# Performance work log

Hardware: AMD Instinct MI355X
Metric: run time of the kernel (lower is better)

Reference implementation:

```python
import jax, jax.numpy as jnp
import numpy as np

NUM_HEADS = 16


def setup_inputs() -> dict:
    key = jax.random.key(0)
    k1, k2, k3, k4 = jax.random.split(key, 4)
    B, N, C = 4, 2048, 1024
    x = jax.random.normal(k1, (B, N, C), dtype=jnp.float32)
    # binary window mask (0/1) as float, shape [B, N, 1]
    mWin = jnp.round(jax.random.uniform(k2, (B, N, 1), dtype=jnp.float32))
    qkv_w = jax.random.normal(k3, (3 * C, C), dtype=jnp.float32) * (C ** -0.5)
    proj_w = jax.random.normal(k4, (C, C), dtype=jnp.float32) * (C ** -0.5)
    proj_b = jnp.zeros((C,), dtype=jnp.float32)
    return {"x": x, "mWin": mWin, "qkv_w": qkv_w, "proj_w": proj_w, "proj_b": proj_b}


def reference(x, mWin, qkv_w, proj_w, proj_b):
    B, N, C = x.shape
    H = NUM_HEADS
    hd = C // H
    scale = hd ** -0.5
    qkv = (x @ qkv_w.T).reshape(B, N, 3, H, hd).transpose(2, 0, 3, 1, 4)
    q, k, v = qkv[0], qkv[1], qkv[2]
    q = q * scale
    m = mWin[:, None]              # [B,1,N,1], broadcasts over heads
    q = q * m
    k = k * m
    v = v * m
    attn = jax.nn.softmax(jnp.einsum('bhqd,bhkd->bhqk', q, k), axis=-1)
    out = jnp.einsum('bhqk,bhkd->bhqd', attn, v)  # [B,H,N,hd]
    out = out.transpose(0, 2, 1, 3).reshape(B, N, C)
    # mx = ((m @ m^T) @ m) = m * sum(m^2) since m is [N,1]; identical math, no NxN buffer
    mx = mWin * jnp.sum(mWin * mWin, axis=1, keepdims=True)  # [B,N,1]
    out = out / (mx + 1e-6)
    return out @ proj_w.T + proj_b
```

## Files before the change

### kernel.cpp

```cpp
#include <hip/hip_runtime.h>

typedef __attribute__((ext_vector_type(8))) short short8v;
typedef __attribute__((ext_vector_type(4))) float f32x4;
typedef __attribute__((ext_vector_type(4))) unsigned short us4;

#define MFMA(a,b,c) __builtin_amdgcn_mfma_f32_16x16x32_bf16(a,b,c,0,0,0)

__device__ __forceinline__ unsigned short f2b(float f){
  unsigned int u = __float_as_uint(f);
  u += 0x7fffu + ((u >> 16) & 1u);
  return (unsigned short)(u >> 16);
}

__device__ __forceinline__ void gll16(const void* g, void* l){
  __builtin_amdgcn_global_load_lds((const __attribute__((address_space(1))) void*)g,
                                   (__attribute__((address_space(3))) void*)l, 16, 0, 0);
}

__device__ __forceinline__ unsigned int cvtpk(float lo, float hi){
  unsigned int r;
  asm("v_cvt_pk_bf16_f32 %0, %1, %2" : "=v"(r) : "v"(lo), "v"(hi));
  return r;
}
__device__ __forceinline__ void pl32swap(unsigned int &a, unsigned int &b){
  asm("v_permlane32_swap_b32 %0, %1" : "+v"(a), "+v"(b));
}
__device__ __forceinline__ void pl16swap(unsigned int &a, unsigned int &b){
  asm("v_permlane16_swap_b32 %0, %1" : "+v"(a), "+v"(b));
}

union U8 { unsigned int u[4]; short8v v; };

__global__ __launch_bounds__(256) void prep_k(
    const float* __restrict__ x, const float* __restrict__ qkv_w,
    const float* __restrict__ proj_w, const float* __restrict__ mWin,
    unsigned short* __restrict__ xb, unsigned short* __restrict__ wqkvb,
    unsigned short* __restrict__ wprojb, float* __restrict__ cnt){
  int blk = blockIdx.x, tid = threadIdx.x;
  const float* src; unsigned short* dst; int base;
  if (blk < 8192){ src = x; dst = xb; base = 0; }
  else if (blk < 11264){ src = qkv_w; dst = wqkvb; base = 8192; }
  else if (blk < 12288){ src = proj_w; dst = wprojb; base = 11264; }
  else {
    int b = blk - 12288;
    float s = 0.f;
    for (int i = tid; i < 2048; i += 256){ float m = mWin[b*2048 + i]; s += m*m; }
    #pragma unroll
    for (int o = 32; o >= 1; o >>= 1) s += __shfl_xor(s, o, 64);
    if ((tid & 63) == 0) atomicAdd(&cnt[b], s);
    return;
  }
  int i = (blk - base)*256 + tid;
  float4 v = reinterpret_cast<const float4*>(src)[i];
  us4 o; o.x = f2b(v.x); o.y = f2b(v.y); o.z = f2b(v.z); o.w = f2b(v.w);
  reinterpret_cast<us4*>(dst)[i] = o;
}

__global__ __launch_bounds__(256,2) void qkv_gemm(
    const unsigned short* __restrict__ xb,
    const unsigned short* __restrict__ wb,
    const float* __restrict__ mWin,
    unsigned short* __restrict__ qb,
    unsigned short* __restrict__ kb,
    unsigned short* __restrict__ vb)
{
  __shared__ unsigned short As[128*64];
  __shared__ unsigned short Bs[128*64];
  int lin = blockIdx.x;
  int swz = (lin & 7) * 192 + (lin >> 3);
  int tM = swz & 63, tN = swz >> 6;
  int tid = threadIdx.x, lane = tid & 63, wv = tid >> 6;
  int lr = lane & 15, lg = lane >> 4;

  const unsigned short* ga[4]; const unsigned short* gbp[4];
  char* lA[4]; char* lB[4];
  #pragma unroll
  for (int c = 0; c < 4; ++c){
    int o = c*4096 + wv*1024 + lane*16;
    int row = o >> 7, cole = (o & 127) >> 1;
    ga[c]  = xb + (tM*128 + row)*1024 + cole;
    gbp[c] = wb + (tN*128 + row)*1024 + cole;
    lA[c] = (char*)As + c*4096 + wv*1024;
    lB[c] = (char*)Bs + c*4096 + wv*1024;
  }

  f32x4 acc[4][4];
  #pragma unroll
  for (int i = 0; i < 4; ++i)
    #pragma unroll
    for (int j = 0; j < 4; ++j) acc[i][j] = (f32x4){0.f,0.f,0.f,0.f};

  int wr = (wv >> 1) * 64, wc = (wv & 1) * 64;

  for (int it = 0; it < 16; ++it){
    #pragma unroll
    for (int c = 0; c < 4; ++c){
      gll16(ga[c]  + it*64, lA[c]);
      gll16(gbp[c] + it*64, lB[c]);
    }
    __syncthreads();
    short8v af[4][2], bf[4][2];
    #pragma unroll
    for (int mi = 0; mi < 4; ++mi)
      #pragma unroll
      for (int ks = 0; ks < 2; ++ks)
        af[mi][ks] = *(const short8v*)&As[(wr + mi*16 + lr)*64 + ks*32 + lg*8];
    #pragma unroll
    for (int ni = 0; ni < 4; ++ni)
      #pragma unroll
      for (int ks = 0; ks < 2; ++ks)
        bf[ni][ks] = *(const short8v*)&Bs[(wc + ni*16 + lr)*64 + ks*32 + lg*8];
    #pragma unroll
    for (int mi = 0; mi < 4; ++mi)
      #pragma unroll
      for (int ni = 0; ni < 4; ++ni)
        #pragma unroll
        for (int ks = 0; ks < 2; ++ks)
          acc[mi][ni] = MFMA(af[mi][ks], bf[ni][ks], acc[mi][ni]);
    __syncthreads();
  }

  int which = tN >> 3;
  int c0 = (tN & 7) * 128;
  if (which == 2){
    #pragma unroll
    for (int mi = 0; mi < 4; ++mi){
      int m0 = tM*128 + wr + mi*16 + lg*4;
      int b = m0 >> 11, n0 = m0 & 2047;
      float f0 = mWin[m0], f1 = mWin[m0+1], f2 = mWin[m0+2], f3 = mWin[m0+3];
      #pragma unroll
      for (int ni = 0; ni < 4; ++ni){
        int col = c0 + wc + ni*16 + lr;
        int h = col >> 6, d = col & 63;
        us4 o;
        o.x = f2b(acc[mi][ni][0] * f0); o.y = f2b(acc[mi][ni][1] * f1);
        o.z = f2b(acc[mi][ni][2] * f2); o.w = f2b(acc[mi][ni][3] * f3);
        *(us4*)&vb[(((b << 4) + h)*64 + d)*2048 + n0] = o;
      }
    }
  } else {
    float sf = (which == 0) ? 0.18033688f : 1.0f;
    unsigned short* dst = (which == 0) ? qb : kb;
    #pragma unroll
    for (int mi = 0; mi < 4; ++mi){
      #pragma unroll
      for (int j = 0; j < 4; ++j){
        int m = tM*128 + wr + mi*16 + lg*4 + j;
        float f = sf * mWin[m];
        int b = m >> 11, n = m & 2047;
        #pragma unroll
        for (int ni = 0; ni < 4; ++ni){
          int col = c0 + wc + ni*16 + lr;
          int h = col >> 6, d = col & 63;
          dst[(((b << 4) + h)*2048 + n)*64 + d] = f2b(acc[mi][ni][j] * f);
        }
      }
    }
  }
}

#define TILE_BODY(CUR, TNEXT, NXT, DO_PF)                                              \
  {                                                                                    \
    if (DO_PF){                                                                        \
      _Pragma("unroll")                                                                \
      for (int r = 0; r < 2; ++r){                                                     \
        gll16(Kg + (TNEXT)*8192 + srow[r]*128 + so[r], ldsK + (NXT)*8192 + r*4096 + wv*1024); \
        gll16(Vg + srow[r]*4096 + (TNEXT)*128 + so[r], ldsV + (NXT)*8192 + r*4096 + wv*1024); \
      }                                                                                \
    }                                                                                  \
    short8v kf[4][2];                                                                  \
    _Pragma("unroll")                                                                  \
    for (int ni = 0; ni < 4; ++ni){                                                    \
      kf[ni][0] = *(const short8v*)(kv0 + (CUR)*8192 + ni*2048);                       \
      kf[ni][1] = *(const short8v*)(kv1 + (CUR)*8192 + ni*2048);                       \
    }                                                                                  \
    f32x4 s[4][4];                                                                     \
    __builtin_amdgcn_s_setprio(1);                                                     \
    _Pragma("unroll")                                                                  \
    for (int mi = 0; mi < 4; ++mi)                                                     \
      _Pragma("unroll")                                                                \
      for (int ni = 0; ni < 4; ++ni){                                                  \
        f32x4 sa = (f32x4){0.f,0.f,0.f,0.f};                                           \
        sa = MFMA(kf[ni][0], qf[mi][0], sa);                                           \
        sa = MFMA(kf[ni][1], qf[mi][1], sa);                                           \
        s[mi][ni] = sa;                                                                \
      }                                                                                \
    __builtin_amdgcn_s_setprio(0);                                                     \
    short8v vf[4][2];                                                                  \
    _Pragma("unroll")                                                                  \
    for (int ni = 0; ni < 4; ++ni){                                                    \
      vf[ni][0] = *(const short8v*)(vv0 + (CUR)*8192 + ni*2048);                       \
      vf[ni][1] = *(const short8v*)(vv1 + (CUR)*8192 + ni*2048);                       \
    }                                                                                  \
    _Pragma("unroll")                                                                  \
    for (int mi = 0; mi < 4; ++mi){                                                    \
      unsigned int R[4][2];                                                            \
      float dl = 0.f;                                                                  \
      _Pragma("unroll")                                                                \
      for (int ni = 0; ni < 4; ++ni){                                                  \
        _Pragma("unroll")                                                              \
        for (int hh = 0; hh < 2; ++hh){                                                \
          float p0 = __builtin_amdgcn_exp2f(s[mi][ni][2*hh]);                          \
          float p1 = __builtin_amdgcn_exp2f(s[mi][ni][2*hh+1]);                        \
          dl += p0 + p1;                                                               \
          R[ni][hh] = cvtpk(p0, p1);                                                   \
        }                                                                              \
      }                                                                                \
      den[mi] += dl;                                                                   \
      pl32swap(R[0][0], R[1][0]); pl16swap(R[0][0], R[1][0]);                          \
      pl32swap(R[0][1], R[1][1]); pl16swap(R[0][1], R[1][1]);                          \
      pl32swap(R[2][0], R[3][0]); pl16swap(R[2][0], R[3][0]);                          \
      pl32swap(R[2][1], R[3][1]); pl16swap(R[2][1], R[3][1]);                          \
      U8 pa0, pa1;                                                                     \
      pa0.u[0] = R[0][0]; pa0.u[1] = R[0][1]; pa0.u[2] = R[1][0]; pa0.u[3] = R[1][1];  \
      pa1.u[0] = R[2][0]; pa1.u[1] = R[2][1]; pa1.u[2] = R[3][0]; pa1.u[3] = R[3][1];  \
      __builtin_amdgcn_s_setprio(1);                                                   \
      _Pragma("unroll")                                                                \
      for (int nf = 0; nf < 4; ++nf){                                                  \
        oacc[mi][nf] = MFMA(pa0.v, vf[nf][0], oacc[mi][nf]);                           \
        oacc[mi][nf] = MFMA(pa1.v, vf[nf][1], oacc[mi][nf]);                           \
      }                                                                                \
      __builtin_amdgcn_s_setprio(0);                                                   \
    }                                                                                  \
    __syncthreads();                                                                   \
  }

__global__ __launch_bounds__(256,2) void attn_k(
  const unsigned short* __restrict__ qbuf,
  const unsigned short* __restrict__ kbuf,
  const unsigned short* __restrict__ vbuf,
  const float* __restrict__ mWin,
  const float* __restrict__ cnt,
  unsigned short* __restrict__ ab)
{
  __shared__ unsigned short Ks[2][4096];
  __shared__ unsigned short Vt[2][4096];
  int lin = blockIdx.x;
  int xcd = lin & 7, slot = lin >> 3;
  int qt = slot & 7;
  int bh = xcd + ((slot >> 3) << 3);
  int b = bh >> 4, h = bh & 15;
  const unsigned short* Q  = qbuf + (bh*2048 + qt*256)*64;
  const char* Kg = (const char*)(kbuf + bh*2048*64);
  const char* Vg = (const char*)(vbuf + bh*64*2048);
  char* ldsK = (char*)Ks; char* ldsV = (char*)Vt;
  int tid = threadIdx.x, lane = tid & 63, wv = tid >> 6;
  int lr = lane & 15, lg = lane >> 4;

  int so[2], srow[2];
  #pragma unroll
  for (int r = 0; r < 2; ++r){
    int o = r*4096 + wv*1024 + lane*16;
    srow[r] = o >> 7;
    so[r] = (o & 127) ^ ((srow[r] & 7) << 4);
  }

  int lb  = lr*128 + ((lg*16) ^ ((lr&3)<<4));
  int ksA = (lr & 4) << 4;
  const char* kv0 = ldsK + lb + ksA;
  const char* kv1 = ldsK + lb + (64 - ksA);
  const char* vv0 = ldsV + lb + ksA;
  const char* vv1 = ldsV + lb + (64 - ksA);

  short8v qf[4][2];
  #pragma unroll
  for (int mi = 0; mi < 4; ++mi)
    #pragma unroll
    for (int ks = 0; ks < 2; ++ks)
      qf[mi][ks] = *(const short8v*)&Q[(wv*64 + mi*16 + lr)*64 + ks*32 + lg*8];

  f32x4 oacc[4][4];
  #pragma unroll
  for (int mi = 0; mi < 4; ++mi)
    #pragma unroll
    for (int nf = 0; nf < 4; ++nf) oacc[mi][nf] = (f32x4){0.f,0.f,0.f,0.f};
  float den[4] = {0.f, 0.f, 0.f, 0.f};

  #pragma unroll
  for (int r = 0; r < 2; ++r){
    gll16(Kg + srow[r]*128  + so[r], ldsK + r*4096 + wv*1024);
    gll16(Vg + srow[r]*4096 + so[r], ldsV + r*4096 + wv*1024);
  }
  __syncthreads();

  #pragma unroll 1
  for (int tt = 0; tt < 16; ++tt){
    int t0 = tt << 1;
    TILE_BODY(0, t0+1, 1, 1)
    TILE_BODY(1, t0+2, 0, (tt < 15))
  }

  #pragma unroll
  for (int mi = 0; mi < 4; ++mi){
    float d = den[mi];
    d += __shfl_xor(d, 16, 64);
    d += __shfl_xor(d, 32, 64);
    den[mi] = d;
  }
  #pragma unroll
  for (int mi = 0; mi < 4; ++mi){
    #pragma unroll
    for (int j = 0; j < 4; ++j){
      float dd = __shfl(den[mi], lg*4 + j, 64);
      int n = qt*256 + wv*64 + mi*16 + lg*4 + j;
      float mv = mWin[b*2048 + n];
      float g = 1.0f / (dd * (mv * cnt[b] + 1e-6f));
      #pragma unroll
      for (int nf = 0; nf < 4; ++nf)
        ab[(b*2048 + n)*1024 + h*64 + nf*16 + lr] = f2b(oacc[mi][nf][j] * g);
    }
  }
}

__global__ __launch_bounds__(256,2) void proj_gemm(
    const unsigned short* __restrict__ abuf,
    const unsigned short* __restrict__ wb,
    const float* __restrict__ pb,
    float* __restrict__ out)
{
  __shared__ unsigned short As[128*64];
  __shared__ unsigned short Bs[128*64];
  int lin = blockIdx.x;
  int swz = (lin & 7) * 64 + (lin >> 3);
  int tM = swz & 63, tN = swz >> 6;
  int tid = threadIdx.x, lane = tid & 63, wv = tid >> 6;
  int lr = lane & 15, lg = lane >> 4;

  const unsigned short* ga[4]; const unsigned short* gbp[4];
  char* lA[4]; char* lB[4];
  #pragma unroll
  for (int c = 0; c < 4; ++c){
    int o = c*4096 + wv*1024 + lane*16;
    int row = o >> 7, cole = (o & 127) >> 1;
    ga[c]  = abuf + (tM*128 + row)*1024 + cole;
    gbp[c] = wb   + (tN*128 + row)*1024 + cole;
    lA[c] = (char*)As + c*4096 + wv*1024;
    lB[c] = (char*)Bs + c*4096 + wv*1024;
  }

  f32x4 acc[4][4];
  #pragma unroll
  for (int i = 0; i < 4; ++i)
    #pragma unroll
    for (int j = 0; j < 4; ++j) acc[i][j] = (f32x4){0.f,0.f,0.f,0.f};

  int wr = (wv >> 1) * 64, wc = (wv & 1) * 64;

  for (int it = 0; it < 16; ++it){
    #pragma unroll
    for (int c = 0; c < 4; ++c){
      gll16(ga[c]  + it*64, lA[c]);
      gll16(gbp[c] + it*64, lB[c]);
    }
    __syncthreads();
    short8v af[4][2], bf[4][2];
    #pragma unroll
    for (int mi = 0; mi < 4; ++mi)
      #pragma unroll
      for (int ks = 0; ks < 2; ++ks)
        af[mi][ks] = *(const short8v*)&As[(wr + mi*16 + lr)*64 + ks*32 + lg*8];
    #pragma unroll
    for (int ni = 0; ni < 4; ++ni)
      #pragma unroll
      for (int ks = 0; ks < 2; ++ks)
        bf[ni][ks] = *(const short8v*)&Bs[(wc + ni*16 + lr)*64 + ks*32 + lg*8];
    #pragma unroll
    for (int mi = 0; mi < 4; ++mi)
      #pragma unroll
      for (int ni = 0; ni < 4; ++ni)
        #pragma unroll
        for (int ks = 0; ks < 2; ++ks)
          acc[mi][ni] = MFMA(af[mi][ks], bf[ni][ks], acc[mi][ni]);
    __syncthreads();
  }

  #pragma unroll
  for (int mi = 0; mi < 4; ++mi){
    #pragma unroll
    for (int j = 0; j < 4; ++j){
      int m = tM*128 + wr + mi*16 + lg*4 + j;
      #pragma unroll
      for (int ni = 0; ni < 4; ++ni){
        int col = tN*128 + wc + ni*16 + lr;
        out[m*1024 + col] = acc[mi][ni][j] + pb[col];
      }
    }
  }
}

extern "C" void kernel_launch(void* const* d_in, const int* in_sizes, int n_in,
                              void* d_out, int out_size, void* d_ws, size_t ws_size,
                              hipStream_t stream) {
  const float* x      = (const float*)d_in[0];
  const float* mWin   = (const float*)d_in[1];
  const float* qkv_w  = (const float*)d_in[2];
  const float* proj_w = (const float*)d_in[3];
  const float* proj_b = (const float*)d_in[4];
  float* out = (float*)d_out;
  char* ws = (char*)d_ws;

  unsigned short* xb     = (unsigned short*)(ws);
  unsigned short* ab     = (unsigned short*)(ws);
  unsigned short* wqkvb  = (unsigned short*)(ws + 16777216);
  unsigned short* wprojb = (unsigned short*)(ws + 23068672);
  unsigned short* qb     = (unsigned short*)(ws + 25165824);
  unsigned short* kb     = (unsigned short*)(ws + 41943040);
  unsigned short* vb     = (unsigned short*)(ws + 58720256);
  float* cnt             = (float*)(ws + 75497472);

  hipMemsetAsync(cnt, 0, 16, stream);
  prep_k<<<12292, 256, 0, stream>>>(x, qkv_w, proj_w, mWin, xb, wqkvb, wprojb, cnt);
  qkv_gemm<<<1536, 256, 0, stream>>>(xb, wqkvb, mWin, qb, kb, vb);
  attn_k<<<512, 256, 0, stream>>>(qb, kb, vb, mWin, cnt, ab);
  proj_gemm<<<512, 256, 0, stream>>>(ab, wprojb, proj_b, out);
}
```

Baseline: 197.3 us.

## Split attention over two key halves with separate combine kernel

The attention kernel now splits the key/value sequence into two halves, so twice as many blocks each process half the keys. Each block writes an unnormalised bf16 partial output and its partial softmax denominators. A new combine kernel adds the two partials, applies the denominator and mask normalisation, and writes the bf16 input to the projection GEMM. The aim is more parallelism in attention. The cost is an extra launch, about three extra full-size activation passes through memory, and an extra bf16 rounding of the partials.

```diff
diff --git a/kernel.cpp b/kernel.cpp
--- a/kernel.cpp
+++ b/kernel.cpp
@@ -10,6 +10,9 @@
   unsigned int u = __float_as_uint(f);
   u += 0x7fffu + ((u >> 16) & 1u);
   return (unsigned short)(u >> 16);
+}
+__device__ __forceinline__ float b2f(unsigned short u){
+  return __uint_as_float(((unsigned int)u) << 16);
 }
 
 __device__ __forceinline__ void gll16(const void* g, void* l){
@@ -229,20 +232,23 @@
   const unsigned short* __restrict__ qbuf,
   const unsigned short* __restrict__ kbuf,
   const unsigned short* __restrict__ vbuf,
-  const float* __restrict__ mWin,
-  const float* __restrict__ cnt,
-  unsigned short* __restrict__ ab)
+  unsigned short* __restrict__ pO0,
+  unsigned short* __restrict__ pO1,
+  float* __restrict__ dn)
 {
   __shared__ unsigned short Ks[2][4096];
   __shared__ unsigned short Vt[2][4096];
   int lin = blockIdx.x;
   int xcd = lin & 7, slot = lin >> 3;
   int qt = slot & 7;
-  int bh = xcd + ((slot >> 3) << 3);
+  int sk = (slot >> 3) & 1;
+  int bh = xcd + ((slot >> 4) << 3);
   int b = bh >> 4, h = bh & 15;
   const unsigned short* Q  = qbuf + (bh*2048 + qt*256)*64;
-  const char* Kg = (const char*)(kbuf + bh*2048*64);
-  const char* Vg = (const char*)(vbuf + bh*64*2048);
+  const char* Kg = (const char*)(kbuf + bh*2048*64) + sk*131072;
+  const char* Vg = (const char*)(vbuf + bh*64*2048) + sk*2048;
+  unsigned short* po = sk ? pO1 : pO0;
+  float* dno = dn + sk*131072 + bh*2048;
   char* ldsK = (char*)Ks; char* ldsV = (char*)Vt;
   int tid = threadIdx.x, lane = tid & 63, wv = tid >> 6;
   int lr = lane & 15, lg = lane >> 4;
@@ -284,10 +290,10 @@
   __syncthreads();
 
   #pragma unroll 1
-  for (int tt = 0; tt < 16; ++tt){
+  for (int tt = 0; tt < 8; ++tt){
     int t0 = tt << 1;
     TILE_BODY(0, t0+1, 1, 1)
-    TILE_BODY(1, t0+2, 0, (tt < 15))
+    TILE_BODY(1, t0+2, 0, (tt < 7))
   }
 
   #pragma unroll
@@ -295,21 +301,40 @@
     float d = den[mi];
     d += __shfl_xor(d, 16, 64);
     d += __shfl_xor(d, 32, 64);
-    den[mi] = d;
+    if (lg == 0) dno[qt*256 + wv*64 + mi*16 + lr] = d;
   }
   #pragma unroll
   for (int mi = 0; mi < 4; ++mi){
     #pragma unroll
     for (int j = 0; j < 4; ++j){
-      float dd = __shfl(den[mi], lg*4 + j, 64);
       int n = qt*256 + wv*64 + mi*16 + lg*4 + j;
-      float mv = mWin[b*2048 + n];
-      float g = 1.0f / (dd * (mv * cnt[b] + 1e-6f));
       #pragma unroll
       for (int nf = 0; nf < 4; ++nf)
-        ab[(b*2048 + n)*1024 + h*64 + nf*16 + lr] = f2b(oacc[mi][nf][j] * g);
-    }
-  }
+        po[(b*2048 + n)*1024 + h*64 + nf*16 + lr] = f2b(oacc[mi][nf][j]);
+    }
+  }
+}
+
+__global__ __launch_bounds__(256) void combine_k(
+    const unsigned short* __restrict__ pO0, const unsigned short* __restrict__ pO1,
+    const float* __restrict__ dn, const float* __restrict__ mWin,
+    const float* __restrict__ cnt, unsigned short* __restrict__ ab)
+{
+  int m = blockIdx.x;
+  int b = m >> 11, n = m & 2047;
+  int col = threadIdx.x * 4;
+  int h = col >> 6;
+  int bh = (b << 4) + h;
+  float den = dn[bh*2048 + n] + dn[131072 + bh*2048 + n];
+  float g = 1.0f / (den * (mWin[m] * cnt[b] + 1e-6f));
+  us4 a = *(const us4*)&pO0[m*1024 + col];
+  us4 c = *(const us4*)&pO1[m*1024 + col];
+  us4 o;
+  o.x = f2b((b2f(a.x) + b2f(c.x)) * g);
+  o.y = f2b((b2f(a.y) + b2f(c.y)) * g);
+  o.z = f2b((b2f(a.z) + b2f(c.z)) * g);
+  o.w = f2b((b2f(a.w) + b2f(c.w)) * g);
+  *(us4*)&ab[m*1024 + col] = o;
 }
 
 __global__ __launch_bounds__(256,2) void proj_gemm(
@@ -400,17 +425,21 @@
   char* ws = (char*)d_ws;
 
   unsigned short* xb     = (unsigned short*)(ws);
-  unsigned short* ab     = (unsigned short*)(ws);
+  unsigned short* pO0    = (unsigned short*)(ws);
   unsigned short* wqkvb  = (unsigned short*)(ws + 16777216);
+  float*          dn     = (float*)(ws + 16777216);
   unsigned short* wprojb = (unsigned short*)(ws + 23068672);
   unsigned short* qb     = (unsigned short*)(ws + 25165824);
+  unsigned short* ab     = (unsigned short*)(ws + 25165824);
   unsigned short* kb     = (unsigned short*)(ws + 41943040);
   unsigned short* vb     = (unsigned short*)(ws + 58720256);
   float* cnt             = (float*)(ws + 75497472);
+  unsigned short* pO1    = (unsigned short*)d_out;
 
   hipMemsetAsync(cnt, 0, 16, stream);
   prep_k<<<12292, 256, 0, stream>>>(x, qkv_w, proj_w, mWin, xb, wqkvb, wprojb, cnt);
   qkv_gemm<<<1536, 256, 0, stream>>>(xb, wqkvb, mWin, qb, kb, vb);
-  attn_k<<<512, 256, 0, stream>>>(qb, kb, vb, mWin, cnt, ab);
+  attn_k<<<1024, 256, 0, stream>>>(qb, kb, vb, pO0, pO1, dn);
+  combine_k<<<8192, 256, 0, stream>>>(pO0, pO1, dn, mWin, cnt, ab);
   proj_gemm<<<512, 256, 0, stream>>>(ab, wprojb, proj_b, out);
 }
```

Measured after the change: 205.3 us. +4.1%, slower.
